# Kernel tuning notes

Hardware: AMD Instinct MI355X
Metric: run time of the kernel (lower is better)

Reference implementation:

```python
import jax, jax.numpy as jnp
import numpy as np

OUT, IN = 4096, 4096
NNZ = 838860  # 0.05 * OUT * IN
ALPHA = 1.0   # set_privacy(True)


def setup_inputs() -> dict:
    key = jax.random.key(0)
    k1, k2, k3, k4, k5, k6 = jax.random.split(key, 6)
    x = jax.random.normal(k1, (2, 2048, IN), dtype=jnp.float32)
    # packed uint4 pairs stored as bytes (kept in int32 per spec; values in [0,256))
    base_packed = jax.random.randint(k2, (OUT, IN // 2), 0, 256, dtype=jnp.int32)
    # per-row dequant scales (positive, small, like ceiling/7)
    scales = jax.random.uniform(k3, (OUT, 1), dtype=jnp.float32, minval=1e-3, maxval=5e-2)
    ortho_vals = jax.random.normal(k4, (NNZ,), dtype=jnp.float32) * 0.02
    ortho_rows = jax.random.randint(k5, (NNZ,), 0, OUT, dtype=jnp.int32)
    ortho_cols = jax.random.randint(k6, (NNZ,), 0, IN, dtype=jnp.int32)
    return {"x": x, "base_packed": base_packed, "scales": scales,
            "ortho_vals": ortho_vals, "ortho_rows": ortho_rows, "ortho_cols": ortho_cols}


def _dequant(base_packed, scales):
    # unpack two int4 values per byte: col 2k <- low nibble, col 2k+1 <- high nibble
    p = base_packed.astype(jnp.int32)
    low = p & 0xF
    high = (p >> 4) & 0xF
    O, K = p.shape
    w_int4 = jnp.stack([low, high], axis=-1).reshape(O, 2 * K) - 8  # offset-binary -> [-8, 7]
    return w_int4.astype(jnp.float32) * scales  # [O, I]


def reference(x, base_packed, scales, ortho_vals, ortho_rows, ortho_cols):
    O = base_packed.shape[0]
    I = 2 * base_packed.shape[1]
    w_base = _dequant(base_packed, scales)  # [O, I] fp32
    # sparse outlier residual scattered into dense weight (CSR spmm equivalent)
    w_corr = jnp.zeros((O, I), jnp.float32).at[ortho_rows, ortho_cols].add(ortho_vals)
    w = w_base + ALPHA * w_corr
    x_flat = x.reshape(-1, I).astype(jnp.float32)
    out = x_flat @ w.T  # [N, O]
    return out.reshape(x.shape[:-1] + (O,)).astype(x.dtype)
```

## Files before the change

### kernel.cpp

```cpp
#include <hip/hip_runtime.h>
#include <cstdint>
#include <cstddef>

typedef __bf16 bf16x8 __attribute__((ext_vector_type(8)));
typedef float f32x4 __attribute__((ext_vector_type(4)));
typedef unsigned short ushort8 __attribute__((ext_vector_type(8)));

#define OUT_DIM 4096
#define IN_DIM 4096
#define NT 64


__device__ __forceinline__ unsigned short f2bf(float f) {
  unsigned u = __float_as_uint(f);
  return (unsigned short)((u + 0x7FFFu + ((u >> 16) & 1u)) >> 16);
}

__device__ __forceinline__ void async_copy16(const void* g, void* l) {
  __builtin_amdgcn_global_load_lds(
      (const __attribute__((address_space(1))) unsigned int*)g,
      (__attribute__((address_space(3))) unsigned int*)l, 16, 0, 0);
}


__global__ __launch_bounds__(256) void dequant_kernel(
    const int* __restrict__ packed, const float* __restrict__ scales,
    unsigned short* __restrict__ wb) {
  int idx = blockIdx.x * 256 + threadIdx.x;
  int4 p = reinterpret_cast<const int4*>(packed)[idx];
  float s = scales[idx >> 9];
  ushort8 o;
  o[0] = f2bf((float)((p.x & 15) - 8) * s);
  o[1] = f2bf((float)(((p.x >> 4) & 15) - 8) * s);
  o[2] = f2bf((float)((p.y & 15) - 8) * s);
  o[3] = f2bf((float)(((p.y >> 4) & 15) - 8) * s);
  o[4] = f2bf((float)((p.z & 15) - 8) * s);
  o[5] = f2bf((float)(((p.z >> 4) & 15) - 8) * s);
  o[6] = f2bf((float)((p.w & 15) - 8) * s);
  o[7] = f2bf((float)(((p.w >> 4) & 15) - 8) * s);
  *reinterpret_cast<ushort8*>(&wb[(size_t)idx * 8]) = o;
}

__global__ __launch_bounds__(256) void scatter_bf16_kernel(
    const float* __restrict__ vals, const int* __restrict__ rows,
    const int* __restrict__ cols, unsigned short* __restrict__ wb, int nnz) {
  int i = blockIdx.x * 256 + threadIdx.x;
  if (i >= nnz) return;
  size_t idx = (size_t)rows[i] * IN_DIM + cols[i];
  unsigned int* word = (unsigned int*)(wb + (idx & ~(size_t)1));
  const bool hi = (idx & 1) != 0;
  const float v = vals[i];
  unsigned int old = *word, assumed;
  do {
    assumed = old;
    unsigned short h = hi ? (unsigned short)(assumed >> 16)
                          : (unsigned short)(assumed & 0xFFFFu);
    float f = __uint_as_float((unsigned)h << 16);
    unsigned short nh = f2bf(f + v);
    unsigned int nw = hi ? ((assumed & 0x0000FFFFu) | ((unsigned)nh << 16))
                         : ((assumed & 0xFFFF0000u) | (unsigned)nh);
    old = atomicCAS(word, assumed, nw);
  } while (old != assumed);
}

__global__ __launch_bounds__(256) void cvt_kernel(
    const float* __restrict__ in, unsigned short* __restrict__ out) {
  int i = blockIdx.x * 256 + threadIdx.x;
  float4 a = reinterpret_cast<const float4*>(in)[2 * i];
  float4 b = reinterpret_cast<const float4*>(in)[2 * i + 1];
  ushort8 o;
  o[0] = f2bf(a.x); o[1] = f2bf(a.y); o[2] = f2bf(a.z); o[3] = f2bf(a.w);
  o[4] = f2bf(b.x); o[5] = f2bf(b.y); o[6] = f2bf(b.z); o[7] = f2bf(b.w);
  *reinterpret_cast<ushort8*>(&out[(size_t)i * 8]) = o;
}


#define SB(buf, op, kh) ((((buf) * 4) + ((op) * 2) + (kh)) * 16384)

#define STAGE(buf, op, kh, kt)                                              \
  do {                                                                      \
    const unsigned short* gsrc_ =                                           \
        (op) ? (const unsigned short*)((const char*)gA + dBA) : gA;         \
    const unsigned short* g_ = gsrc_ + (kt) * 64 + (kh) * 32;               \
    unsigned short* l_ =                                                    \
        (unsigned short*)((char*)lds + SB(buf, op, kh)) + wave * 512;       \
    async_copy16(g_, l_);                                                   \
    async_copy16(g_ + 128 * IN_DIM, l_ + 4096);                             \
  } while (0)

#define MFMA_ __builtin_amdgcn_mfma_f32_16x16x32_bf16

#define LDA4(d0, d1, d2, d3, BUF, KS, MH)                                   \
  d0 = *(const bf16x8*)(ldsc + (laneA + SB(BUF, 0, KS) + (MH) * 4096 + 0)); \
  d1 = *(const bf16x8*)(ldsc + (laneA + SB(BUF, 0, KS) + (MH) * 4096 + 1024)); \
  d2 = *(const bf16x8*)(ldsc + (laneA + SB(BUF, 0, KS) + (MH) * 4096 + 2048)); \
  d3 = *(const bf16x8*)(ldsc + (laneA + SB(BUF, 0, KS) + (MH) * 4096 + 3072))

#define LDB4(d0, d1, d2, d3, BUF, KS)                                       \
  d0 = *(const bf16x8*)(ldsc + (laneB + SB(BUF, 1, KS) + 0));               \
  d1 = *(const bf16x8*)(ldsc + (laneB + SB(BUF, 1, KS) + 1024));            \
  d2 = *(const bf16x8*)(ldsc + (laneB + SB(BUF, 1, KS) + 2048));            \
  d3 = *(const bf16x8*)(ldsc + (laneB + SB(BUF, 1, KS) + 3072))

#define MM16(MH, A0, A1, A2, A3, B0, B1, B2, B3)                            \
  acc[(MH) * 4 + 0][0] = MFMA_(A0, B0, acc[(MH) * 4 + 0][0], 0, 0, 0);      \
  acc[(MH) * 4 + 0][1] = MFMA_(A0, B1, acc[(MH) * 4 + 0][1], 0, 0, 0);      \
  acc[(MH) * 4 + 0][2] = MFMA_(A0, B2, acc[(MH) * 4 + 0][2], 0, 0, 0);      \
  acc[(MH) * 4 + 0][3] = MFMA_(A0, B3, acc[(MH) * 4 + 0][3], 0, 0, 0);      \
  acc[(MH) * 4 + 1][0] = MFMA_(A1, B0, acc[(MH) * 4 + 1][0], 0, 0, 0);      \
  acc[(MH) * 4 + 1][1] = MFMA_(A1, B1, acc[(MH) * 4 + 1][1], 0, 0, 0);      \
  acc[(MH) * 4 + 1][2] = MFMA_(A1, B2, acc[(MH) * 4 + 1][2], 0, 0, 0);      \
  acc[(MH) * 4 + 1][3] = MFMA_(A1, B3, acc[(MH) * 4 + 1][3], 0, 0, 0);      \
  acc[(MH) * 4 + 2][0] = MFMA_(A2, B0, acc[(MH) * 4 + 2][0], 0, 0, 0);      \
  acc[(MH) * 4 + 2][1] = MFMA_(A2, B1, acc[(MH) * 4 + 2][1], 0, 0, 0);      \
  acc[(MH) * 4 + 2][2] = MFMA_(A2, B2, acc[(MH) * 4 + 2][2], 0, 0, 0);      \
  acc[(MH) * 4 + 2][3] = MFMA_(A2, B3, acc[(MH) * 4 + 2][3], 0, 0, 0);      \
  acc[(MH) * 4 + 3][0] = MFMA_(A3, B0, acc[(MH) * 4 + 3][0], 0, 0, 0);      \
  acc[(MH) * 4 + 3][1] = MFMA_(A3, B1, acc[(MH) * 4 + 3][1], 0, 0, 0);      \
  acc[(MH) * 4 + 3][2] = MFMA_(A3, B2, acc[(MH) * 4 + 3][2], 0, 0, 0);      \
  acc[(MH) * 4 + 3][3] = MFMA_(A3, B3, acc[(MH) * 4 + 3][3], 0, 0, 0)

#define PHASEX(STAGEST, DOWAIT, LGN, MH, A0, A1, A2, A3, B0, B1, B2, B3, ...) \
  do {                                                                      \
    STAGEST;                                                                \
    if (DOWAIT) asm volatile("s_waitcnt vmcnt(8)" ::: "memory");            \
    __builtin_amdgcn_s_barrier();                                           \
    __VA_ARGS__;                                                            \
    __builtin_amdgcn_sched_barrier(0);                                      \
    asm volatile("s_waitcnt lgkmcnt(" #LGN ")" ::: "memory");               \
    __builtin_amdgcn_sched_barrier(0);                                      \
    __builtin_amdgcn_s_setprio(1);                                          \
    MM16(MH, A0, A1, A2, A3, B0, B1, B2, B3);                               \
    __builtin_amdgcn_s_setprio(0);                                          \
    __builtin_amdgcn_s_barrier();                                           \
  } while (0)

#define MINC(x) ((x) < NT ? (x) : (NT - 1))

#define TILE(BUF, t)                                                        \
  do {                                                                      \
    PHASEX(STAGE(1 - (BUF), 0, 1, MINC((t) + 1)), 0, 4, 0,                  \
           aE0, aE1, aE2, aE3, bE0, bE1, bE2, bE3,                          \
           LDA4(aO0, aO1, aO2, aO3, BUF, 0, 1));                            \
    PHASEX(STAGE(1 - (BUF), 1, 1, MINC((t) + 1)), 1, 8, 1,                  \
           aO0, aO1, aO2, aO3, bE0, bE1, bE2, bE3,                          \
           LDA4(aE0, aE1, aE2, aE3, BUF, 1, 0);                             \
           LDB4(bO0, bO1, bO2, bO3, BUF, 1));                               \
    PHASEX(STAGE(BUF, 0, 0, MINC((t) + 2)), 0, 4, 0,                        \
           aE0, aE1, aE2, aE3, bO0, bO1, bO2, bO3,                          \
           LDA4(aO0, aO1, aO2, aO3, BUF, 1, 1));                            \
    PHASEX(STAGE(BUF, 1, 0, MINC((t) + 2)), 1, 8, 1,                        \
           aO0, aO1, aO2, aO3, bO0, bO1, bO2, bO3,                          \
           LDA4(aE0, aE1, aE2, aE3, 1 - (BUF), 0, 0);                       \
           LDB4(bE0, bE1, bE2, bE3, 1 - (BUF), 0));                         \
  } while (0)

__global__ __launch_bounds__(512, 2) void gemm_kernel(
    const unsigned short* __restrict__ A,
    const unsigned short* __restrict__ B,
    float* __restrict__ C) {
  __shared__ __align__(16) unsigned short lds[65536];
  const char* ldsc = (const char*)lds;

  const int bid = blockIdx.x;
  const int xcd = bid & 7, i_ = bid >> 3;
  const int bm = (xcd >> 1) * 4 + (i_ >> 3);
  const int bn = (xcd & 1) * 8 + (i_ & 7);
  const int m0 = bm * 256, n0 = bn * 256;

  const int tid = threadIdx.x;
  const int wave = tid >> 6, lane = tid & 63;
  const int wm = wave >> 2, wn = wave & 3;
  const int lrow = lane & 15, lk = lane >> 4;

  const int r0 = tid >> 2, s0 = tid & 3;
  const int s0s = s0 ^ ((r0 >> 1) & 3);
  const unsigned short* gA = A + (size_t)(m0 + r0) * IN_DIM + s0s * 8;
  const ptrdiff_t dBA = ((const char*)B - (const char*)A) +
                        (ptrdiff_t)(n0 - m0) * IN_DIM * 2;

  const int lks = lk ^ ((lrow >> 1) & 3);
  const int laneA = (wm * 128 + lrow) * 64 + lks * 16;
  const int laneB = (wn * 64 + lrow) * 64 + lks * 16;

  f32x4 acc[8][4];
#pragma unroll
  for (int mi = 0; mi < 8; ++mi)
#pragma unroll
    for (int ni = 0; ni < 4; ++ni) acc[mi][ni] = (f32x4){0.f, 0.f, 0.f, 0.f};

  bf16x8 aE0, aE1, aE2, aE3, aO0, aO1, aO2, aO3;
  bf16x8 bE0, bE1, bE2, bE3, bO0, bO1, bO2, bO3;

  STAGE(0, 0, 0, 0); STAGE(0, 1, 0, 0);
  asm volatile("" ::: "memory");
  STAGE(0, 0, 1, 0); STAGE(0, 1, 1, 0);
  asm volatile("" ::: "memory");
  STAGE(1, 0, 0, 1); STAGE(1, 1, 0, 1);
  asm volatile("s_waitcnt vmcnt(8)" ::: "memory");
  __builtin_amdgcn_s_barrier();

  LDA4(aE0, aE1, aE2, aE3, 0, 0, 0);
  LDB4(bE0, bE1, bE2, bE3, 0, 0);

#pragma unroll 1
  for (int p = 0; p < NT / 2; ++p) {
    const int te = 2 * p;
    TILE(0, te);
    TILE(1, te + 1);
  }
  asm volatile("s_waitcnt vmcnt(0) lgkmcnt(0)" ::: "memory");

#pragma unroll
  for (int mi = 0; mi < 8; ++mi)
#pragma unroll
    for (int ni = 0; ni < 4; ++ni) {
      int m = m0 + wm * 128 + mi * 16 + lk * 4;
      int n = n0 + wn * 64 + ni * 16 + lrow;
      float* cp = &C[(size_t)m * OUT_DIM + n];
#pragma unroll
      for (int r = 0; r < 4; ++r) cp[(size_t)r * OUT_DIM] = acc[mi][ni][r];
    }
}


extern "C" void kernel_launch(void* const* d_in, const int* in_sizes, int n_in,
                              void* d_out, int out_size, void* d_ws, size_t ws_size,
                              hipStream_t stream) {
  const float* x      = (const float*)d_in[0];
  const int*   packed = (const int*)d_in[1];
  const float* scales = (const float*)d_in[2];
  const float* vals   = (const float*)d_in[3];
  const int*   rows   = (const int*)d_in[4];
  const int*   cols   = (const int*)d_in[5];
  float* out = (float*)d_out;

  const int nnz = in_sizes[3];

  char* ws = (char*)d_ws;
  const size_t MB = 1024 * 1024;
  unsigned short* Wb = (unsigned short*)ws;
  unsigned short* Xb = (unsigned short*)(ws + 32 * MB);

  dequant_kernel<<<8192, 256, 0, stream>>>(packed, scales, Wb);
  scatter_bf16_kernel<<<(nnz + 255) / 256, 256, 0, stream>>>(vals, rows, cols, Wb, nnz);
  cvt_kernel<<<8192, 256, 0, stream>>>(x, Xb);
  gemm_kernel<<<256, 512, 0, stream>>>(Xb, Wb, out);
}
```

Before: 188.2 us.

## Drop LDS-to-register prefetch ping-pong; load fragments just before each MFMA phase

```diff
diff --git a/kernel.cpp b/kernel.cpp
--- a/kernel.cpp
+++ b/kernel.cpp
@@ -120,39 +120,43 @@
   acc[(MH) * 4 + 3][2] = MFMA_(A3, B2, acc[(MH) * 4 + 3][2], 0, 0, 0);      \
   acc[(MH) * 4 + 3][3] = MFMA_(A3, B3, acc[(MH) * 4 + 3][3], 0, 0, 0)
 
-#define PHASEX(STAGEST, DOWAIT, LGN, MH, A0, A1, A2, A3, B0, B1, B2, B3, ...) \
-  do {                                                                      \
+#define PHASE8(BUF, KS, MH, STAGEST, DOWAIT)                                \
+  do {                                                                      \
+    bf16x8 a0_, a1_, a2_, a3_;                                              \
+    LDA4(a0_, a1_, a2_, a3_, BUF, KS, MH);                                  \
+    LDB4(bB0, bB1, bB2, bB3, BUF, KS);                                      \
     STAGEST;                                                                \
     if (DOWAIT) asm volatile("s_waitcnt vmcnt(8)" ::: "memory");            \
     __builtin_amdgcn_s_barrier();                                           \
-    __VA_ARGS__;                                                            \
-    __builtin_amdgcn_sched_barrier(0);                                      \
-    asm volatile("s_waitcnt lgkmcnt(" #LGN ")" ::: "memory");               \
-    __builtin_amdgcn_sched_barrier(0);                                      \
+    asm volatile("s_waitcnt lgkmcnt(0)" ::: "memory");                      \
     __builtin_amdgcn_s_setprio(1);                                          \
-    MM16(MH, A0, A1, A2, A3, B0, B1, B2, B3);                               \
+    MM16(MH, a0_, a1_, a2_, a3_, bB0, bB1, bB2, bB3);                       \
     __builtin_amdgcn_s_setprio(0);                                          \
     __builtin_amdgcn_s_barrier();                                           \
   } while (0)
 
+#define PHASE4(BUF, KS, MH, STAGEST, DOWAIT)                                \
+  do {                                                                      \
+    bf16x8 a0_, a1_, a2_, a3_;                                              \
+    LDA4(a0_, a1_, a2_, a3_, BUF, KS, MH);                                  \
+    STAGEST;                                                                \
+    if (DOWAIT) asm volatile("s_waitcnt vmcnt(8)" ::: "memory");            \
+    __builtin_amdgcn_s_barrier();                                           \
+    asm volatile("s_waitcnt lgkmcnt(0)" ::: "memory");                      \
+    __builtin_amdgcn_s_setprio(1);                                          \
+    MM16(MH, a0_, a1_, a2_, a3_, bB0, bB1, bB2, bB3);                       \
+    __builtin_amdgcn_s_setprio(0);                                          \
+    __builtin_amdgcn_s_barrier();                                           \
+  } while (0)
+
 #define MINC(x) ((x) < NT ? (x) : (NT - 1))
 
 #define TILE(BUF, t)                                                        \
   do {                                                                      \
-    PHASEX(STAGE(1 - (BUF), 0, 1, MINC((t) + 1)), 0, 4, 0,                  \
-           aE0, aE1, aE2, aE3, bE0, bE1, bE2, bE3,                          \
-           LDA4(aO0, aO1, aO2, aO3, BUF, 0, 1));                            \
-    PHASEX(STAGE(1 - (BUF), 1, 1, MINC((t) + 1)), 1, 8, 1,                  \
-           aO0, aO1, aO2, aO3, bE0, bE1, bE2, bE3,                          \
-           LDA4(aE0, aE1, aE2, aE3, BUF, 1, 0);                             \
-           LDB4(bO0, bO1, bO2, bO3, BUF, 1));                               \
-    PHASEX(STAGE(BUF, 0, 0, MINC((t) + 2)), 0, 4, 0,                        \
-           aE0, aE1, aE2, aE3, bO0, bO1, bO2, bO3,                          \
-           LDA4(aO0, aO1, aO2, aO3, BUF, 1, 1));                            \
-    PHASEX(STAGE(BUF, 1, 0, MINC((t) + 2)), 1, 8, 1,                        \
-           aO0, aO1, aO2, aO3, bO0, bO1, bO2, bO3,                          \
-           LDA4(aE0, aE1, aE2, aE3, 1 - (BUF), 0, 0);                       \
-           LDB4(bE0, bE1, bE2, bE3, 1 - (BUF), 0));                         \
+    PHASE8(BUF, 0, 0, STAGE(1 - (BUF), 0, 1, MINC((t) + 1)), 0);            \
+    PHASE4(BUF, 0, 1, STAGE(1 - (BUF), 1, 1, MINC((t) + 1)), 1);            \
+    PHASE8(BUF, 1, 0, STAGE(BUF, 0, 0, MINC((t) + 2)), 0);                  \
+    PHASE4(BUF, 1, 1, STAGE(BUF, 1, 0, MINC((t) + 2)), 1);                  \
   } while (0)
 
 __global__ __launch_bounds__(512, 2) void gemm_kernel(
@@ -189,8 +193,7 @@
 #pragma unroll
     for (int ni = 0; ni < 4; ++ni) acc[mi][ni] = (f32x4){0.f, 0.f, 0.f, 0.f};
 
-  bf16x8 aE0, aE1, aE2, aE3, aO0, aO1, aO2, aO3;
-  bf16x8 bE0, bE1, bE2, bE3, bO0, bO1, bO2, bO3;
+  bf16x8 bB0, bB1, bB2, bB3;
 
   STAGE(0, 0, 0, 0); STAGE(0, 1, 0, 0);
   asm volatile("" ::: "memory");
@@ -199,9 +202,6 @@
   STAGE(1, 0, 0, 1); STAGE(1, 1, 0, 1);
   asm volatile("s_waitcnt vmcnt(8)" ::: "memory");
   __builtin_amdgcn_s_barrier();
-
-  LDA4(aE0, aE1, aE2, aE3, 0, 0, 0);
-  LDB4(bE0, bE1, bE2, bE3, 0, 0);
 
 #pragma unroll 1
   for (int p = 0; p < NT / 2; ++p) {
```

New measurement: 185.1 us. Within noise of the previous version (-1.6%).
